# Optimization experiments

Hardware: AMD Instinct MI355X
Metric: run time of the kernel (lower is better)

The kernel has to match this reference:

```python
import jax, jax.numpy as jnp
import numpy as np

EMBED = 1024
HEADS = 16
B, T = 4, 2048


def setup_inputs() -> dict:
    key = jax.random.key(0)
    k1, k2, k3, k4, k5 = jax.random.split(key, 5)
    s_in = 1.0 / np.sqrt(EMBED)
    return {
        "x": jax.random.normal(k1, (B, T, EMBED), dtype=jnp.float32),
        "w_qkv": jax.random.uniform(k2, (3 * EMBED, EMBED), jnp.float32, -s_in, s_in),
        "b_qkv": jax.random.uniform(k3, (3 * EMBED,), jnp.float32, -s_in, s_in),
        "w_proj": jax.random.uniform(k4, (EMBED, EMBED), jnp.float32, -s_in, s_in),
        "b_proj": jax.random.uniform(k5, (EMBED,), jnp.float32, -s_in, s_in),
    }


def reference(x, w_qkv, b_qkv, w_proj, b_proj):
    Bz, Tz, C = x.shape
    nh = HEADS
    hs = C // nh
    qkv = jnp.einsum('btc,oc->bto', x, w_qkv) + b_qkv  # [B,T,3C]
    q, k, v = jnp.split(qkv, 3, axis=-1)
    # [B, nh, T, hs]
    q = q.reshape(Bz, Tz, nh, hs).transpose(0, 2, 1, 3)
    k = k.reshape(Bz, Tz, nh, hs).transpose(0, 2, 1, 3)
    v = v.reshape(Bz, Tz, nh, hs).transpose(0, 2, 1, 3)
    scale = 1.0 / np.sqrt(hs).astype(np.float32)
    att = jnp.einsum('bhqd,bhkd->bhqk', q, k) * scale
    causal_mask = jnp.tril(jnp.ones((Tz, Tz), dtype=bool))
    att = jnp.where(causal_mask[None, None], att, jnp.finfo(att.dtype).min)
    att = jax.nn.softmax(att, axis=-1)
    y = jnp.einsum('bhqk,bhkd->bhqd', att, v)
    y = y.transpose(0, 2, 1, 3).reshape(Bz, Tz, C)
    return jnp.einsum('btc,oc->bto', y, w_proj) + b_proj
```

## Files before the change

### kernel.cpp

```cpp
#include <hip/hip_runtime.h>

typedef __bf16 bf16x8 __attribute__((ext_vector_type(8)));
typedef float f32x4 __attribute__((ext_vector_type(4)));

#define DI __device__ __forceinline__

#define WAIT_VMCNT(N)                                        \
  do {                                                       \
    __builtin_amdgcn_sched_barrier(0);                       \
    asm volatile("s_waitcnt vmcnt(" #N ")" ::: "memory");    \
    __builtin_amdgcn_sched_barrier(0);                       \
  } while (0)

DI unsigned short f2bf(float f) {
  unsigned int u = __float_as_uint(f);
  u += 0x7FFFu + ((u >> 16) & 1u);
  return (unsigned short)(u >> 16);
}

DI unsigned cvt_pk_bf16(float a, float b) {
  unsigned r;
  asm("v_cvt_pk_bf16_f32 %0, %1, %2" : "=v"(r) : "v"(a), "v"(b));
  return r;
}

DI float exp2_fast(float x) {
  float r;
  asm("v_exp_f32 %0, %1" : "=v"(r) : "v"(x));
  return r;
}

DI void fence() { asm volatile("" ::: "memory"); }
DI void bar() { fence(); __builtin_amdgcn_s_barrier(); fence(); }

DI bf16x8 ld16(const void* p) {
  union { uint4 u; bf16x8 b; } c;
  c.u = *reinterpret_cast<const uint4*>(p);
  return c.b;
}

DI f32x4 mfma16(bf16x8 a, bf16x8 b, f32x4 c) {
  return __builtin_amdgcn_mfma_f32_16x16x32_bf16(a, b, c, 0, 0, 0);
}

DI void gload_lds16(const void* g, void* l) {
  __builtin_amdgcn_global_load_lds(
      (const __attribute__((address_space(1))) unsigned int*)g,
      (__attribute__((address_space(3))) unsigned int*)l, 16, 0, 0);
}

__global__ void cvt_all(const float* __restrict__ x, const float* __restrict__ wq,
                        const float* __restrict__ wp,
                        unsigned short* __restrict__ xb, unsigned short* __restrict__ wqb,
                        unsigned short* __restrict__ wpb) {
  int i = blockIdx.x * blockDim.x + threadIdx.x;
  const float* s;
  unsigned short* d;
  int off;
  if (i < 2097152) { s = x; d = xb; off = i; }
  else if (i < 2097152 + 786432) { s = wq; d = wqb; off = i - 2097152; }
  else { s = wp; d = wpb; off = i - (2097152 + 786432); }
  float4 v = reinterpret_cast<const float4*>(s)[off];
  uint2 o;
  o.x = cvt_pk_bf16(v.x, v.y);
  o.y = cvt_pk_bf16(v.z, v.w);
  reinterpret_cast<uint2*>(d)[off] = o;
}

template <int N, int MODE>
__global__ __launch_bounds__(256)
void gemm_bt(const unsigned short* __restrict__ A,
             const unsigned short* __restrict__ W,
             const float* __restrict__ bias,
             float* __restrict__ out,
             unsigned short* __restrict__ qo,
             unsigned short* __restrict__ ko,
             unsigned short* __restrict__ vo) {
  constexpr int K = 1024;
  __shared__ __align__(16) char smem[32768];
  char* Asm = smem;
  char* Bsm = smem + 16384;
  const int tid = threadIdx.x;
  const int ln = tid & 63;
  const int w  = tid >> 6;
  const int wm = w >> 1, wn = w & 1;
  const int g = ln >> 4, q = ln & 15;
  const int m0 = blockIdx.x * 128;
  const int n0 = blockIdx.y * 128;

  f32x4 acc[4][4] = {};

  for (int kt = 0; kt < K / 64; ++kt) {
    if (kt) bar();
#pragma unroll
    for (int i = 0; i < 4; ++i) {
      const int chunk = i * 4 + w;
      const int o = chunk * 1024 + ln * 16;
      const int row = o >> 7;
      const int colb = (o & 127) ^ ((row & 7) << 4);
      gload_lds16((const char*)A + ((size_t)(m0 + row) * K + kt * 64) * 2 + colb,
                  Asm + chunk * 1024);
      gload_lds16((const char*)W + ((size_t)(n0 + row) * K + kt * 64) * 2 + colb,
                  Bsm + chunk * 1024);
    }
    WAIT_VMCNT(0);
    bar();
#pragma unroll
    for (int ks = 0; ks < 2; ++ks) {
      bf16x8 av[4], bv[4];
#pragma unroll
      for (int mf = 0; mf < 4; ++mf) {
        const int row = wm * 64 + mf * 16 + q;
        av[mf] = ld16(Asm + ((row * 128 + ks * 64 + g * 16) ^ ((row & 7) << 4)));
      }
#pragma unroll
      for (int nf = 0; nf < 4; ++nf) {
        const int row = wn * 64 + nf * 16 + q;
        bv[nf] = ld16(Bsm + ((row * 128 + ks * 64 + g * 16) ^ ((row & 7) << 4)));
      }
#pragma unroll
      for (int mf = 0; mf < 4; ++mf)
#pragma unroll
        for (int nf = 0; nf < 4; ++nf)
          acc[mf][nf] = mfma16(av[mf], bv[nf], acc[mf][nf]);
    }
  }

#pragma unroll
  for (int nf = 0; nf < 4; ++nf) {
    const int col = n0 + wn * 64 + nf * 16 + q;
    const float bv = bias[col];
#pragma unroll
    for (int mf = 0; mf < 4; ++mf) {
      const int rbase = m0 + wm * 64 + mf * 16 + g * 4;
      if constexpr (MODE == 0) {
#pragma unroll
        for (int r = 0; r < 4; ++r)
          out[(size_t)(rbase + r) * N + col] = acc[mf][nf][r] + bv;
      } else {
        const int b = rbase >> 11, t0 = rbase & 2047;
        if (col < 1024) {
          const int h = col >> 6, d = col & 63;
          unsigned short* qp = qo + ((((size_t)b * 16 + h) << 11) + t0) * 64 + d;
#pragma unroll
          for (int r = 0; r < 4; ++r)
            qp[r * 64] = f2bf((acc[mf][nf][r] + bv) * 0.18033688011112042f);
        } else if (col < 2048) {
          const int c = col - 1024;
          const int h = c >> 6, d = c & 63;
          unsigned short* kp = ko + ((((size_t)b * 16 + h) << 11) + t0) * 64 + d;
#pragma unroll
          for (int r = 0; r < 4; ++r)
            kp[r * 64] = f2bf(acc[mf][nf][r] + bv);
        } else {
          const int c = col - 2048;
          const int h = c >> 6, d = c & 63;
          uint2 pk;
          pk.x = cvt_pk_bf16(acc[mf][nf][0] + bv, acc[mf][nf][1] + bv);
          pk.y = cvt_pk_bf16(acc[mf][nf][2] + bv, acc[mf][nf][3] + bv);
          *(uint2*)(vo + ((((size_t)b * 16 + h) << 6) + d) * 2048 + t0) = pk;
        }
      }
    }
  }
}

__global__ __launch_bounds__(256)
void attn_fwd(const unsigned short* __restrict__ Qb,
              const unsigned short* __restrict__ Kb,
              const unsigned short* __restrict__ Vtb,
              unsigned short* __restrict__ Yb) {
  __shared__ __align__(16) char smem[49152];
  char* Psm = smem + 32768;
  const int tid = threadIdx.x;
  const int ln = tid & 63;
  const int w = tid >> 6;
  const int g = ln >> 4, q = ln & 15;
  const int bh = blockIdx.x;
  const int pair = blockIdx.y;
  const size_t base = (size_t)bh * 2048 * 64;
  const int b = bh >> 4, h = bh & 15;

  auto stage = [&](int j, int buf) {
    char* Kd = smem + buf * 16384;
    char* Vd = Kd + 8192;
    const int kv0 = j << 6;
    const char* Kg = (const char*)(Kb + base + (size_t)kv0 * 64);
    const char* Vg = (const char*)(Vtb + base) + kv0 * 2;
#pragma unroll
    for (int i = 0; i < 2; ++i) {
      const int chunk = i * 4 + w;
      const int o = chunk * 1024 + ln * 16;
      const int row = o >> 7;
      const int colb = (o & 127) ^ ((row & 7) << 4);
      gload_lds16(Kg + row * 128 + colb, Kd + chunk * 1024);
      gload_lds16(Vg + (size_t)row * 4096 + colb, Vd + chunk * 1024);
    }
  };

  auto run_qtile = [&](int qt) {
    const int q0 = qt * 128;
    const int qw = q0 + w * 32;

    bf16x8 qf[2][2];
#pragma unroll
    for (int nf = 0; nf < 2; ++nf)
#pragma unroll
      for (int kf = 0; kf < 2; ++kf)
        qf[nf][kf] = ld16(Qb + base + (size_t)(qw + nf * 16 + q) * 64 + kf * 32 + g * 8);
    WAIT_VMCNT(0);

    float m_run[2] = {-INFINITY, -INFINITY};
    float l_run[2] = {0.f, 0.f};
    f32x4 yt[4][2] = {};

    const int nkv = (q0 >> 6) + 2;
    stage(0, 0);
    for (int j = 0; j < nkv; ++j) {
      if (j + 1 < nkv) {
        stage(j + 1, (j + 1) & 1);
        WAIT_VMCNT(4);
      } else {
        WAIT_VMCNT(0);
      }
      bar();

      const int kv0 = j << 6;
      const char* Ksm = smem + (j & 1) * 16384;
      const char* Vsm = Ksm + 8192;
      const bool active = (kv0 <= qw + 31);
      if (active) {
        f32x4 st[4][2] = {};
        __builtin_amdgcn_s_setprio(1);
#pragma unroll
        for (int mf = 0; mf < 4; ++mf) {
          const int row = mf * 16 + q;
          const int swz = (row & 7) << 4;
          const bf16x8 a0 = ld16(Ksm + ((row * 128 + g * 16) ^ swz));
          const bf16x8 a1 = ld16(Ksm + ((row * 128 + 64 + g * 16) ^ swz));
#pragma unroll
          for (int nf = 0; nf < 2; ++nf) {
            st[mf][nf] = mfma16(a0, qf[nf][0], st[mf][nf]);
            st[mf][nf] = mfma16(a1, qf[nf][1], st[mf][nf]);
          }
        }
        __builtin_amdgcn_s_setprio(0);
        if (kv0 + 63 > qw) {
#pragma unroll
          for (int mf = 0; mf < 4; ++mf)
#pragma unroll
            for (int nf = 0; nf < 2; ++nf)
#pragma unroll
              for (int r = 0; r < 4; ++r)
                if (kv0 + mf * 16 + g * 4 + r > qw + nf * 16 + q)
                  st[mf][nf][r] = -INFINITY;
        }
#pragma unroll
        for (int nf = 0; nf < 2; ++nf) {
          float vmax = -INFINITY;
#pragma unroll
          for (int mf = 0; mf < 4; ++mf) {
            const f32x4 v = st[mf][nf];
            vmax = fmaxf(fmaxf(vmax, fmaxf(v[0], v[1])), fmaxf(v[2], v[3]));
          }
          vmax = fmaxf(vmax, __shfl_xor(vmax, 16));
          vmax = fmaxf(vmax, __shfl_xor(vmax, 32));
          const float mo = m_run[nf];
          if (__any(vmax > mo)) {
            const float mn = fmaxf(mo, vmax);
            const float corr = exp2_fast(mo - mn);
            m_run[nf] = mn;
            l_run[nf] *= corr;
#pragma unroll
            for (int mfd = 0; mfd < 4; ++mfd) yt[mfd][nf] *= corr;
          }
          const float mcur = m_run[nf];
          float ls = 0.f;
#pragma unroll
          for (int mf = 0; mf < 4; ++mf) {
            f32x4 p;
#pragma unroll
            for (int r = 0; r < 4; ++r) p[r] = exp2_fast(st[mf][nf][r] - mcur);
            ls += (p[0] + p[1]) + (p[2] + p[3]);
            uint2 pk2;
            pk2.x = cvt_pk_bf16(p[0], p[1]);
            pk2.y = cvt_pk_bf16(p[2], p[3]);
            const int prow = w * 32 + nf * 16 + q;
            *(uint2*)(Psm + ((prow * 128 + mf * 32 + g * 8) ^ ((prow & 7) << 4))) = pk2;
          }
          ls += __shfl_xor(ls, 16);
          ls += __shfl_xor(ls, 32);
          l_run[nf] += ls;
        }
        __builtin_amdgcn_s_setprio(1);
#pragma unroll
        for (int kf = 0; kf < 2; ++kf) {
          bf16x8 pb[2];
#pragma unroll
          for (int nf = 0; nf < 2; ++nf) {
            const int prow = w * 32 + nf * 16 + q;
            pb[nf] = ld16(Psm + ((prow * 128 + kf * 64 + g * 16) ^ ((prow & 7) << 4)));
          }
#pragma unroll
          for (int mfd = 0; mfd < 4; ++mfd) {
            const int vrow = mfd * 16 + q;
            const bf16x8 vv = ld16(Vsm + ((vrow * 128 + kf * 64 + g * 16) ^ ((vrow & 7) << 4)));
#pragma unroll
            for (int nf = 0; nf < 2; ++nf)
              yt[mfd][nf] = mfma16(vv, pb[nf], yt[mfd][nf]);
          }
        }
        __builtin_amdgcn_s_setprio(0);
      }
      bar();
    }

#pragma unroll
    for (int nf = 0; nf < 2; ++nf) {
      const float inv = 1.f / l_run[nf];
      const int qr = qw + nf * 16 + q;
      unsigned short* yp = Yb + (size_t)(b * 2048 + qr) * 1024 + h * 64;
#pragma unroll
      for (int mfd = 0; mfd < 4; ++mfd) {
        uint2 o2;
        o2.x = cvt_pk_bf16(yt[mfd][nf][0] * inv, yt[mfd][nf][1] * inv);
        o2.y = cvt_pk_bf16(yt[mfd][nf][2] * inv, yt[mfd][nf][3] * inv);
        *(uint2*)(yp + mfd * 16 + g * 4) = o2;
      }
    }
  };

  run_qtile(15 - pair);
  run_qtile(pair);
}

extern "C" void kernel_launch(void* const* d_in, const int* in_sizes, int n_in,
                              void* d_out, int out_size, void* d_ws, size_t ws_size,
                              hipStream_t stream) {
  const float* x      = (const float*)d_in[0];
  const float* w_qkv  = (const float*)d_in[1];
  const float* b_qkv  = (const float*)d_in[2];
  const float* w_proj = (const float*)d_in[3];
  const float* b_proj = (const float*)d_in[4];
  float* out = (float*)d_out;
  char* ws = (char*)d_ws;

  unsigned short* xb  = (unsigned short*)(ws);
  unsigned short* wqb = (unsigned short*)(ws + (size_t)(16 << 20));
  unsigned short* wpb = (unsigned short*)(ws + (size_t)(22 << 20));
  unsigned short* Qb  = (unsigned short*)(ws + (size_t)(24 << 20));
  unsigned short* Kb  = (unsigned short*)(ws + (size_t)(40 << 20));
  unsigned short* Vtb = (unsigned short*)(ws + (size_t)(56 << 20));
  unsigned short* Yb  = (unsigned short*)(ws + (size_t)(72 << 20));

  cvt_all<<<12288, 256, 0, stream>>>(x, w_qkv, w_proj, xb, wqb, wpb);
  gemm_bt<3072, 1><<<dim3(64, 24), 256, 0, stream>>>(xb, wqb, b_qkv, nullptr, Qb, Kb, Vtb);
  attn_fwd<<<dim3(64, 8), 256, 0, stream>>>(Qb, Kb, Vtb, Yb);
  gemm_bt<1024, 0><<<dim3(64, 8), 256, 0, stream>>>(Yb, wpb, b_proj, out, nullptr, nullptr, nullptr);
}
```

Before: 174.2 us.

## Halve attention query tile to 64 rows and double grid with per-warp P buffers

Reduces the attention query tile from 128 to 64 rows (16 per warp instead of 32) and doubles the grid to 64x16 blocks, still pairing tiles qt and 31-qt for causal load balance. It shrinks shared memory to 40KB, gives each warp its own P scratch region, and adds occupancy launch bounds of 4. The aim is more blocks in flight, finer causal granularity, and fewer wasted masked tiles. In exchange, each staged K/V tile is reused across fewer query rows, which raises the loads and barriers per unit of MFMA work.

```diff
diff --git a/kernel.cpp b/kernel.cpp
--- a/kernel.cpp
+++ b/kernel.cpp
@@ -165,17 +165,17 @@
   }
 }
 
-__global__ __launch_bounds__(256)
+__global__ __launch_bounds__(256, 4)
 void attn_fwd(const unsigned short* __restrict__ Qb,
               const unsigned short* __restrict__ Kb,
               const unsigned short* __restrict__ Vtb,
               unsigned short* __restrict__ Yb) {
-  __shared__ __align__(16) char smem[49152];
-  char* Psm = smem + 32768;
+  __shared__ __align__(16) char smem[40960];
   const int tid = threadIdx.x;
   const int ln = tid & 63;
   const int w = tid >> 6;
   const int g = ln >> 4, q = ln & 15;
+  char* Psm = smem + 32768 + w * 2048;
   const int bh = blockIdx.x;
   const int pair = blockIdx.y;
   const size_t base = (size_t)bh * 2048 * 64;
@@ -199,22 +199,20 @@
   };
 
   auto run_qtile = [&](int qt) {
-    const int q0 = qt * 128;
-    const int qw = q0 + w * 32;
-
-    bf16x8 qf[2][2];
-#pragma unroll
-    for (int nf = 0; nf < 2; ++nf)
-#pragma unroll
-      for (int kf = 0; kf < 2; ++kf)
-        qf[nf][kf] = ld16(Qb + base + (size_t)(qw + nf * 16 + q) * 64 + kf * 32 + g * 8);
+    const int q0 = qt * 64;
+    const int qw = q0 + w * 16;
+
+    bf16x8 qf[2];
+#pragma unroll
+    for (int kf = 0; kf < 2; ++kf)
+      qf[kf] = ld16(Qb + base + (size_t)(qw + q) * 64 + kf * 32 + g * 8);
     WAIT_VMCNT(0);
 
-    float m_run[2] = {-INFINITY, -INFINITY};
-    float l_run[2] = {0.f, 0.f};
-    f32x4 yt[4][2] = {};
-
-    const int nkv = (q0 >> 6) + 2;
+    float m_run = -INFINITY;
+    float l_run = 0.f;
+    f32x4 yt[4] = {};
+
+    const int nkv = qt + 1;
     stage(0, 0);
     for (int j = 0; j < nkv; ++j) {
       if (j + 1 < nkv) {
@@ -228,109 +226,91 @@
       const int kv0 = j << 6;
       const char* Ksm = smem + (j & 1) * 16384;
       const char* Vsm = Ksm + 8192;
-      const bool active = (kv0 <= qw + 31);
-      if (active) {
-        f32x4 st[4][2] = {};
-        __builtin_amdgcn_s_setprio(1);
+      f32x4 st[4] = {};
+      __builtin_amdgcn_s_setprio(1);
+#pragma unroll
+      for (int mf = 0; mf < 4; ++mf) {
+        const int row = mf * 16 + q;
+        const int swz = (row & 7) << 4;
+        const bf16x8 a0 = ld16(Ksm + ((row * 128 + g * 16) ^ swz));
+        const bf16x8 a1 = ld16(Ksm + ((row * 128 + 64 + g * 16) ^ swz));
+        st[mf] = mfma16(a0, qf[0], st[mf]);
+        st[mf] = mfma16(a1, qf[1], st[mf]);
+      }
+      __builtin_amdgcn_s_setprio(0);
+      if (kv0 + 63 > qw) {
+#pragma unroll
+        for (int mf = 0; mf < 4; ++mf)
+#pragma unroll
+          for (int r = 0; r < 4; ++r)
+            if (kv0 + mf * 16 + g * 4 + r > qw + q)
+              st[mf][r] = -INFINITY;
+      }
+      {
+        float vmax = -INFINITY;
 #pragma unroll
         for (int mf = 0; mf < 4; ++mf) {
-          const int row = mf * 16 + q;
-          const int swz = (row & 7) << 4;
-          const bf16x8 a0 = ld16(Ksm + ((row * 128 + g * 16) ^ swz));
-          const bf16x8 a1 = ld16(Ksm + ((row * 128 + 64 + g * 16) ^ swz));
-#pragma unroll
-          for (int nf = 0; nf < 2; ++nf) {
-            st[mf][nf] = mfma16(a0, qf[nf][0], st[mf][nf]);
-            st[mf][nf] = mfma16(a1, qf[nf][1], st[mf][nf]);
-          }
-        }
-        __builtin_amdgcn_s_setprio(0);
-        if (kv0 + 63 > qw) {
-#pragma unroll
-          for (int mf = 0; mf < 4; ++mf)
-#pragma unroll
-            for (int nf = 0; nf < 2; ++nf)
-#pragma unroll
-              for (int r = 0; r < 4; ++r)
-                if (kv0 + mf * 16 + g * 4 + r > qw + nf * 16 + q)
-                  st[mf][nf][r] = -INFINITY;
-        }
-#pragma unroll
-        for (int nf = 0; nf < 2; ++nf) {
-          float vmax = -INFINITY;
-#pragma unroll
-          for (int mf = 0; mf < 4; ++mf) {
-            const f32x4 v = st[mf][nf];
-            vmax = fmaxf(fmaxf(vmax, fmaxf(v[0], v[1])), fmaxf(v[2], v[3]));
-          }
-          vmax = fmaxf(vmax, __shfl_xor(vmax, 16));
-          vmax = fmaxf(vmax, __shfl_xor(vmax, 32));
-          const float mo = m_run[nf];
-          if (__any(vmax > mo)) {
-            const float mn = fmaxf(mo, vmax);
-            const float corr = exp2_fast(mo - mn);
-            m_run[nf] = mn;
-            l_run[nf] *= corr;
-#pragma unroll
-            for (int mfd = 0; mfd < 4; ++mfd) yt[mfd][nf] *= corr;
-          }
-          const float mcur = m_run[nf];
-          float ls = 0.f;
-#pragma unroll
-          for (int mf = 0; mf < 4; ++mf) {
-            f32x4 p;
-#pragma unroll
-            for (int r = 0; r < 4; ++r) p[r] = exp2_fast(st[mf][nf][r] - mcur);
-            ls += (p[0] + p[1]) + (p[2] + p[3]);
-            uint2 pk2;
-            pk2.x = cvt_pk_bf16(p[0], p[1]);
-            pk2.y = cvt_pk_bf16(p[2], p[3]);
-            const int prow = w * 32 + nf * 16 + q;
-            *(uint2*)(Psm + ((prow * 128 + mf * 32 + g * 8) ^ ((prow & 7) << 4))) = pk2;
-          }
-          ls += __shfl_xor(ls, 16);
-          ls += __shfl_xor(ls, 32);
-          l_run[nf] += ls;
-        }
-        __builtin_amdgcn_s_setprio(1);
-#pragma unroll
-        for (int kf = 0; kf < 2; ++kf) {
-          bf16x8 pb[2];
-#pragma unroll
-          for (int nf = 0; nf < 2; ++nf) {
-            const int prow = w * 32 + nf * 16 + q;
-            pb[nf] = ld16(Psm + ((prow * 128 + kf * 64 + g * 16) ^ ((prow & 7) << 4)));
-          }
-#pragma unroll
-          for (int mfd = 0; mfd < 4; ++mfd) {
-            const int vrow = mfd * 16 + q;
-            const bf16x8 vv = ld16(Vsm + ((vrow * 128 + kf * 64 + g * 16) ^ ((vrow & 7) << 4)));
-#pragma unroll
-            for (int nf = 0; nf < 2; ++nf)
-              yt[mfd][nf] = mfma16(vv, pb[nf], yt[mfd][nf]);
-          }
-        }
-        __builtin_amdgcn_s_setprio(0);
-      }
+          const f32x4 v = st[mf];
+          vmax = fmaxf(fmaxf(vmax, fmaxf(v[0], v[1])), fmaxf(v[2], v[3]));
+        }
+        vmax = fmaxf(vmax, __shfl_xor(vmax, 16));
+        vmax = fmaxf(vmax, __shfl_xor(vmax, 32));
+        const float mo = m_run;
+        if (__any(vmax > mo)) {
+          const float mn = fmaxf(mo, vmax);
+          const float corr = exp2_fast(mo - mn);
+          m_run = mn;
+          l_run *= corr;
+#pragma unroll
+          for (int mfd = 0; mfd < 4; ++mfd) yt[mfd] *= corr;
+        }
+        const float mcur = m_run;
+        float ls = 0.f;
+#pragma unroll
+        for (int mf = 0; mf < 4; ++mf) {
+          f32x4 p;
+#pragma unroll
+          for (int r = 0; r < 4; ++r) p[r] = exp2_fast(st[mf][r] - mcur);
+          ls += (p[0] + p[1]) + (p[2] + p[3]);
+          uint2 pk2;
+          pk2.x = cvt_pk_bf16(p[0], p[1]);
+          pk2.y = cvt_pk_bf16(p[2], p[3]);
+          *(uint2*)(Psm + ((q * 128 + mf * 32 + g * 8) ^ ((q & 7) << 4))) = pk2;
+        }
+        ls += __shfl_xor(ls, 16);
+        ls += __shfl_xor(ls, 32);
+        l_run += ls;
+      }
+      asm volatile("s_waitcnt lgkmcnt(0)" ::: "memory");
+      __builtin_amdgcn_sched_barrier(0);
+      __builtin_amdgcn_s_setprio(1);
+#pragma unroll
+      for (int kf = 0; kf < 2; ++kf) {
+        const bf16x8 pb = ld16(Psm + ((q * 128 + kf * 64 + g * 16) ^ ((q & 7) << 4)));
+#pragma unroll
+        for (int mfd = 0; mfd < 4; ++mfd) {
+          const int vrow = mfd * 16 + q;
+          const bf16x8 vv = ld16(Vsm + ((vrow * 128 + kf * 64 + g * 16) ^ ((vrow & 7) << 4)));
+          yt[mfd] = mfma16(vv, pb, yt[mfd]);
+        }
+      }
+      __builtin_amdgcn_s_setprio(0);
       bar();
     }
 
-#pragma unroll
-    for (int nf = 0; nf < 2; ++nf) {
-      const float inv = 1.f / l_run[nf];
-      const int qr = qw + nf * 16 + q;
-      unsigned short* yp = Yb + (size_t)(b * 2048 + qr) * 1024 + h * 64;
-#pragma unroll
-      for (int mfd = 0; mfd < 4; ++mfd) {
-        uint2 o2;
-        o2.x = cvt_pk_bf16(yt[mfd][nf][0] * inv, yt[mfd][nf][1] * inv);
-        o2.y = cvt_pk_bf16(yt[mfd][nf][2] * inv, yt[mfd][nf][3] * inv);
-        *(uint2*)(yp + mfd * 16 + g * 4) = o2;
-      }
+    const float inv = 1.f / l_run;
+    const int qr = qw + q;
+    unsigned short* yp = Yb + (size_t)(b * 2048 + qr) * 1024 + h * 64;
+#pragma unroll
+    for (int mfd = 0; mfd < 4; ++mfd) {
+      uint2 o2;
+      o2.x = cvt_pk_bf16(yt[mfd][0] * inv, yt[mfd][1] * inv);
+      o2.y = cvt_pk_bf16(yt[mfd][2] * inv, yt[mfd][3] * inv);
+      *(uint2*)(yp + mfd * 16 + g * 4) = o2;
     }
   };
 
-  run_qtile(15 - pair);
+  run_qtile(31 - pair);
   run_qtile(pair);
 }
 
@@ -355,6 +335,6 @@
 
   cvt_all<<<12288, 256, 0, stream>>>(x, w_qkv, w_proj, xb, wqb, wpb);
   gemm_bt<3072, 1><<<dim3(64, 24), 256, 0, stream>>>(xb, wqb, b_qkv, nullptr, Qb, Kb, Vtb);
-  attn_fwd<<<dim3(64, 8), 256, 0, stream>>>(Qb, Kb, Vtb, Yb);
+  attn_fwd<<<dim3(64, 16), 256, 0, stream>>>(Qb, Kb, Vtb, Yb);
   gemm_bt<1024, 0><<<dim3(64, 8), 256, 0, stream>>>(Yb, wpb, b_proj, out, nullptr, nullptr, nullptr);
 }
```

After: 167.0 us. -4.1%, faster.
